# Kernel optimization log

Measured on AMD Instinct MI355X. Metric: run time of the kernel, lower is better.

## Reference

```python
import jax, jax.numpy as jnp
import numpy as np

NUM_CLASSES = 100            # num_classes (no-object class index == NUM_CLASSES)
MIN_PAIR_W = 0.1             # min_point_pair_weight
EPS = 1e-8


def setup_inputs() -> dict:
    key = jax.random.key(0)
    ks = jax.random.split(key, 8)
    B, Q, C1 = 16, 200, NUM_CLASSES + 1
    M = 800                  # matched GT instances across the batch
    NPTS = 200000            # sampled pixel points (per-point query-logit vectors)
    P = 500000               # point pairs for the clustering loss
    pred_logits = jax.random.normal(ks[0], (B, Q, C1), dtype=jnp.float32)
    targets = jax.random.randint(ks[1], (M,), 0, NUM_CLASSES)
    idx_b = jax.random.randint(ks[2], (M,), 0, B)
    idx_q = jax.random.randint(ks[3], (M,), 0, Q)
    src_clusters = jax.random.normal(ks[4], (NPTS, Q), dtype=jnp.float32)
    pairs = jax.random.randint(ks[5], (P, 2), 0, NPTS)
    pair_pos = jax.random.bernoulli(ks[6], 0.5, (P,))
    pair_weights = jax.random.uniform(ks[7], (P,), dtype=jnp.float32)
    # empty_weight buffer: ones with eos_coef on the no-object class
    empty_weight = jnp.ones((C1,), dtype=jnp.float32).at[-1].set(0.1)
    return {"pred_logits": pred_logits, "targets": targets, "idx_b": idx_b,
            "idx_q": idx_q, "src_clusters": src_clusters, "pairs": pairs,
            "pair_pos": pair_pos, "pair_weights": pair_weights,
            "empty_weight": empty_weight}


def _loss_labels(pred_logits, targets, idx_b, idx_q, empty_weight):
    B, Q, _ = pred_logits.shape
    # target_classes = full(no-object); target_classes[indices] = targets
    target_classes = jnp.full((B, Q), NUM_CLASSES, dtype=jnp.int32)
    target_classes = target_classes.at[idx_b, idx_q].set(targets.astype(jnp.int32))
    logp = jax.nn.log_softmax(pred_logits.astype(jnp.float32), axis=-1)  # [B,Q,C+1]
    nll = -jnp.take_along_axis(logp, target_classes[..., None], axis=-1)[..., 0]
    w = empty_weight[target_classes]
    # torch weighted cross_entropy: sum(w*nll)/sum(w)
    return jnp.sum(w * nll) / jnp.sum(w)


def _loss_clusters(src_clusters, pairs, pair_pos, pair_weights):
    a = src_clusters[pairs[:, 0]]            # [P,Q] gather
    b = src_clusters[pairs[:, 1]]            # [P,Q] gather
    cos = jnp.sum(a * b, axis=-1) / (
        jnp.linalg.norm(a, axis=-1) * jnp.linalg.norm(b, axis=-1) + EPS)
    w = jnp.maximum(pair_weights, MIN_PAIR_W)
    per_pair = jnp.where(pair_pos, 1.0 - cos, jnp.maximum(cos, 0.0))
    return jnp.sum(w * per_pair) / jnp.sum(w)


def reference(pred_logits, targets, idx_b, idx_q, src_clusters, pairs,
              pair_pos, pair_weights, empty_weight):
    loss_ce = _loss_labels(pred_logits, targets, idx_b, idx_q, empty_weight)
    loss_cluster = _loss_clusters(src_clusters, pairs, pair_pos, pair_weights)
    return loss_ce + loss_cluster
```

## Files before the change

### kernel.cpp

```cpp
#include <hip/hip_runtime.h>
#include <math.h>

#define NUM_CLASSES_ 100
#define C1_ 101
#define BQ_ 3200
#define QDIM_ 200

__global__ void init_kernel(float* acc, int* tc) {
    int i = blockIdx.x * blockDim.x + threadIdx.x;
    if (i < 4) acc[i] = 0.0f;
    if (i < BQ_) tc[i] = -1;
}

__global__ void scatter_kernel(const int* __restrict__ targets,
                               const int* __restrict__ idx_b,
                               const int* __restrict__ idx_q,
                               int* tc, int M) {
    int m = blockIdx.x * blockDim.x + threadIdx.x;
    if (m < M) {
        int slot = idx_b[m] * QDIM_ + idx_q[m];
        atomicMax(&tc[slot], (m << 8) | targets[m]);
    }
}

__global__ __launch_bounds__(256) void ce_kernel(const float* __restrict__ logits,
                                                 const int* __restrict__ tc,
                                                 const float* __restrict__ empty_w,
                                                 float* acc) {
    int lane = threadIdx.x & 63;
    int gw = (blockIdx.x * blockDim.x + threadIdx.x) >> 6;
    int nw = (gridDim.x * blockDim.x) >> 6;
    float lnum = 0.0f, lden = 0.0f;
    for (int row = gw; row < BQ_; row += nw) {
        const float* x = logits + (size_t)row * C1_;
        float x0 = x[lane];
        bool has2 = (lane < C1_ - 64);
        float x1 = has2 ? x[lane + 64] : -INFINITY;
        float m = fmaxf(x0, x1);
        #pragma unroll
        for (int off = 32; off; off >>= 1) m = fmaxf(m, __shfl_xor(m, off));
        float s = expf(x0 - m) + (has2 ? expf(x1 - m) : 0.0f);
        #pragma unroll
        for (int off = 32; off; off >>= 1) s += __shfl_xor(s, off);
        int packed = tc[row];
        int cls = (packed >= 0) ? (packed & 255) : NUM_CLASSES_;
        float xt = x[cls];
        float nll = -(xt - m - logf(s));
        float w = empty_w[cls];
        lnum += w * nll;
        lden += w;
    }
    if (lane == 0) { atomicAdd(&acc[0], lnum); atomicAdd(&acc[1], lden); }
}

__global__ __launch_bounds__(256) void pair_kernel(const float* __restrict__ src,
                                                   const int* __restrict__ pairs,
                                                   const int* __restrict__ pos,
                                                   const float* __restrict__ pw,
                                                   float* acc, int P) {
    int lane = threadIdx.x & 63;
    int gw = (blockIdx.x * blockDim.x + threadIdx.x) >> 6;
    int nw = (gridDim.x * blockDim.x) >> 6;
    float num = 0.0f, den = 0.0f;
    for (int p = gw; p < P; p += nw) {
        int ia = pairs[2 * p];
        int ib = pairs[2 * p + 1];
        float dot = 0.0f, saa = 0.0f, sbb = 0.0f;
        if (lane < QDIM_ / 4) {
            float4 a = *(reinterpret_cast<const float4*>(src + (size_t)ia * QDIM_) + lane);
            float4 b = *(reinterpret_cast<const float4*>(src + (size_t)ib * QDIM_) + lane);
            dot = a.x * b.x + a.y * b.y + a.z * b.z + a.w * b.w;
            saa = a.x * a.x + a.y * a.y + a.z * a.z + a.w * a.w;
            sbb = b.x * b.x + b.y * b.y + b.z * b.z + b.w * b.w;
        }
        #pragma unroll
        for (int off = 32; off; off >>= 1) {
            dot += __shfl_xor(dot, off);
            saa += __shfl_xor(saa, off);
            sbb += __shfl_xor(sbb, off);
        }
        float cosv = dot / (sqrtf(saa) * sqrtf(sbb) + 1e-8f);
        float per = pos[p] ? (1.0f - cosv) : fmaxf(cosv, 0.0f);
        float w = fmaxf(pw[p], 0.1f);
        num += w * per;
        den += w;
    }
    __shared__ float snum[4], sden[4];
    int wib = threadIdx.x >> 6;
    if (lane == 0) { snum[wib] = num; sden[wib] = den; }
    __syncthreads();
    if (threadIdx.x == 0) {
        float n = snum[0] + snum[1] + snum[2] + snum[3];
        float d = sden[0] + sden[1] + sden[2] + sden[3];
        atomicAdd(&acc[2], n);
        atomicAdd(&acc[3], d);
    }
}

__global__ void final_kernel(const float* __restrict__ acc, float* out) {
    if (threadIdx.x == 0 && blockIdx.x == 0)
        out[0] = acc[0] / acc[1] + acc[2] / acc[3];
}

extern "C" void kernel_launch(void* const* d_in, const int* in_sizes, int n_in,
                              void* d_out, int out_size, void* d_ws, size_t ws_size,
                              hipStream_t stream) {
    const float* pred_logits = (const float*)d_in[0];
    const int*   targets     = (const int*)d_in[1];
    const int*   idx_b       = (const int*)d_in[2];
    const int*   idx_q       = (const int*)d_in[3];
    const float* src         = (const float*)d_in[4];
    const int*   pairs       = (const int*)d_in[5];
    const int*   pair_pos    = (const int*)d_in[6];
    const float* pair_w      = (const float*)d_in[7];
    const float* empty_w     = (const float*)d_in[8];
    float* out = (float*)d_out;

    float* acc = (float*)d_ws;
    int*   tc  = (int*)((char*)d_ws + 16);

    int M = in_sizes[1];
    int P = in_sizes[7];

    init_kernel<<<(BQ_ + 255) / 256, 256, 0, stream>>>(acc, tc);
    scatter_kernel<<<(M + 255) / 256, 256, 0, stream>>>(targets, idx_b, idx_q, tc, M);
    ce_kernel<<<50, 256, 0, stream>>>(pred_logits, tc, empty_w, acc);
    pair_kernel<<<2048, 256, 0, stream>>>(src, pairs, pair_pos, pair_w, acc, P);
    final_kernel<<<1, 64, 0, stream>>>(acc, out);
}
```

Before: 393.1 us.

## Precompute per-point inverse norms and use them in pair cosine kernel

Adds a kernel that computes the inverse L2 norm of each of the 200k point rows once. The pair kernel then only computes the dot product and multiplies by the two cached inverse norms, which removes two squared-sum reductions and the sqrt/divide from each of 500k pairs. It also loads each pair as one int2, unrolls the pair loop by two, and raises the CE kernel grid from 50 to 200 blocks. The cost is a full extra pass over src (about 160MB) plus workspace space for the norms. The EPS term is dropped, so a zero-norm row would give inf/NaN instead of the reference's finite value.

```diff
diff --git a/kernel.cpp b/kernel.cpp
--- a/kernel.cpp
+++ b/kernel.cpp
@@ -53,33 +53,61 @@
     if (lane == 0) { atomicAdd(&acc[0], lnum); atomicAdd(&acc[1], lden); }
 }
 
+__global__ __launch_bounds__(256) void norm_kernel(const float* __restrict__ src,
+                                                   float* __restrict__ invn, int npts) {
+    int lane = threadIdx.x & 63;
+    int gw = (blockIdx.x * blockDim.x + threadIdx.x) >> 6;
+    int nw = (gridDim.x * blockDim.x) >> 6;
+    for (int r = gw; r < npts; r += nw) {
+        float s = 0.0f;
+        if (lane < QDIM_ / 4) {
+            float4 a = reinterpret_cast<const float4*>(src + (size_t)r * QDIM_)[lane];
+            s = a.x * a.x + a.y * a.y + a.z * a.z + a.w * a.w;
+        }
+        #pragma unroll
+        for (int off = 32; off; off >>= 1) s += __shfl_xor(s, off);
+        if (lane == 0) invn[r] = 1.0f / sqrtf(s);
+    }
+}
+
+template <bool PRE>
 __global__ __launch_bounds__(256) void pair_kernel(const float* __restrict__ src,
                                                    const int* __restrict__ pairs,
                                                    const int* __restrict__ pos,
                                                    const float* __restrict__ pw,
+                                                   const float* __restrict__ invn,
                                                    float* acc, int P) {
     int lane = threadIdx.x & 63;
     int gw = (blockIdx.x * blockDim.x + threadIdx.x) >> 6;
     int nw = (gridDim.x * blockDim.x) >> 6;
     float num = 0.0f, den = 0.0f;
+    #pragma unroll 2
     for (int p = gw; p < P; p += nw) {
-        int ia = pairs[2 * p];
-        int ib = pairs[2 * p + 1];
+        int2 pr = reinterpret_cast<const int2*>(pairs)[p];
         float dot = 0.0f, saa = 0.0f, sbb = 0.0f;
         if (lane < QDIM_ / 4) {
-            float4 a = *(reinterpret_cast<const float4*>(src + (size_t)ia * QDIM_) + lane);
-            float4 b = *(reinterpret_cast<const float4*>(src + (size_t)ib * QDIM_) + lane);
+            float4 a = reinterpret_cast<const float4*>(src + (size_t)pr.x * QDIM_)[lane];
+            float4 b = reinterpret_cast<const float4*>(src + (size_t)pr.y * QDIM_)[lane];
             dot = a.x * b.x + a.y * b.y + a.z * b.z + a.w * b.w;
-            saa = a.x * a.x + a.y * a.y + a.z * a.z + a.w * a.w;
-            sbb = b.x * b.x + b.y * b.y + b.z * b.z + b.w * b.w;
+            if (!PRE) {
+                saa = a.x * a.x + a.y * a.y + a.z * a.z + a.w * a.w;
+                sbb = b.x * b.x + b.y * b.y + b.z * b.z + b.w * b.w;
+            }
         }
         #pragma unroll
         for (int off = 32; off; off >>= 1) {
             dot += __shfl_xor(dot, off);
-            saa += __shfl_xor(saa, off);
-            sbb += __shfl_xor(sbb, off);
+            if (!PRE) {
+                saa += __shfl_xor(saa, off);
+                sbb += __shfl_xor(sbb, off);
+            }
         }
-        float cosv = dot / (sqrtf(saa) * sqrtf(sbb) + 1e-8f);
+        float cosv;
+        if (PRE) {
+            cosv = dot * invn[pr.x] * invn[pr.y];
+        } else {
+            cosv = dot / (sqrtf(saa) * sqrtf(sbb) + 1e-8f);
+        }
         float per = pos[p] ? (1.0f - cosv) : fmaxf(cosv, 0.0f);
         float w = fmaxf(pw[p], 0.1f);
         num += w * per;
@@ -90,10 +118,8 @@
     if (lane == 0) { snum[wib] = num; sden[wib] = den; }
     __syncthreads();
     if (threadIdx.x == 0) {
-        float n = snum[0] + snum[1] + snum[2] + snum[3];
-        float d = sden[0] + sden[1] + sden[2] + sden[3];
-        atomicAdd(&acc[2], n);
-        atomicAdd(&acc[3], d);
+        atomicAdd(&acc[2], snum[0] + snum[1] + snum[2] + snum[3]);
+        atomicAdd(&acc[3], sden[0] + sden[1] + sden[2] + sden[3]);
     }
 }
 
@@ -118,13 +144,22 @@
 
     float* acc = (float*)d_ws;
     int*   tc  = (int*)((char*)d_ws + 16);
+    float* invn = (float*)((char*)d_ws + 16384);
 
     int M = in_sizes[1];
     int P = in_sizes[7];
+    int npts = in_sizes[4] / QDIM_;
 
     init_kernel<<<(BQ_ + 255) / 256, 256, 0, stream>>>(acc, tc);
     scatter_kernel<<<(M + 255) / 256, 256, 0, stream>>>(targets, idx_b, idx_q, tc, M);
-    ce_kernel<<<50, 256, 0, stream>>>(pred_logits, tc, empty_w, acc);
-    pair_kernel<<<2048, 256, 0, stream>>>(src, pairs, pair_pos, pair_w, acc, P);
+    ce_kernel<<<200, 256, 0, stream>>>(pred_logits, tc, empty_w, acc);
+
+    bool pre = ws_size >= (size_t)16384 + (size_t)npts * 4;
+    if (pre) {
+        norm_kernel<<<1024, 256, 0, stream>>>(src, invn, npts);
+        pair_kernel<true><<<2048, 256, 0, stream>>>(src, pairs, pair_pos, pair_w, invn, acc, P);
+    } else {
+        pair_kernel<false><<<2048, 256, 0, stream>>>(src, pairs, pair_pos, pair_w, nullptr, acc, P);
+    }
     final_kernel<<<1, 64, 0, stream>>>(acc, out);
 }
```

After: 448.6 us. +14.1%, slower.
